# Optimization experiments

Hardware: AMD Instinct MI355X
Metric: run time of the kernel (lower is better)

The kernel has to match this reference:

```python
import jax, jax.numpy as jnp
import numpy as np

H = 128      # hidden_size
ATT = 128    # attention_size
NS = 1024    # num attendee statements
NE = 512     # num attendee eres
M = 1024     # num attenders


def setup_inputs() -> dict:
    key = jax.random.key(0)
    ks = jax.random.split(key, 16)
    s = 1.0 / np.sqrt(H)
    return {
        'attendee_stmts': jax.random.normal(ks[0], (NS, H), jnp.float32),
        'attendee_eres': jax.random.normal(ks[1], (NE, H), jnp.float32),
        'attender': jax.random.normal(ks[2], (M, H), jnp.float32),
        # Score stmt_to_stmt (concat): Linear(2H->H) then Linear(H->1)
        'Wc_s': jax.random.normal(ks[3], (H, 2 * H), jnp.float32) * s,
        'bc_s': jax.random.normal(ks[4], (H,), jnp.float32) * s,
        'ws_s': jax.random.normal(ks[5], (H,), jnp.float32) * s,
        'bs_s': jax.random.normal(ks[6], (1,), jnp.float32) * s,
        # Score ere_to_stmt (concat)
        'Wc_e': jax.random.normal(ks[7], (H, 2 * H), jnp.float32) * s,
        'bc_e': jax.random.normal(ks[8], (H,), jnp.float32) * s,
        'ws_e': jax.random.normal(ks[9], (H,), jnp.float32) * s,
        'bs_e': jax.random.normal(ks[10], (1,), jnp.float32) * s,
        # Attention combine: Linear(3H -> ATT)
        'W_lin': jax.random.normal(ks[11], (ATT, 3 * H), jnp.float32) * s,
        'b_lin': jax.random.normal(ks[12], (ATT,), jnp.float32) * s,
        # coherence_linear: Linear(ATT -> 1)
        'W_coh': jax.random.normal(ks[13], (1, ATT), jnp.float32) * s,
        'b_coh': jax.random.normal(ks[14], (1,), jnp.float32) * s,
    }


def _concat_score(first, second, Wc, bc, ws, bs):
    # torch: single(tanh(concat(cat([first_i, second_j])))) over all (i, j)
    # split concat weight so we never materialize the [N, M, 2H] concat
    h = first.shape[-1]
    A = first @ Wc[:, :h].T + bc          # [N, H]
    B = second @ Wc[:, h:].T              # [M, H]
    Hnm = jnp.tanh(A[:, None, :] + B[None, :, :])   # [N, M, H]
    return jnp.einsum('nmh,h->nm', Hnm, ws) + bs[0]  # [N, M]


def reference(attendee_stmts, attendee_eres, attender,
              Wc_s, bc_s, ws_s, bs_s,
              Wc_e, bc_e, ws_e, bs_e,
              W_lin, b_lin, W_coh, b_coh):
    # unnormalized scores, softmax over attendees (dim 0)
    w_ss = jax.nn.softmax(_concat_score(attendee_stmts, attender, Wc_s, bc_s, ws_s, bs_s), axis=0)  # [NS, M]
    w_es = jax.nn.softmax(_concat_score(attendee_eres, attender, Wc_e, bc_e, ws_e, bs_e), axis=0)   # [NE, M]
    # context vectors: weights^T @ attendees
    ctx_s = jnp.einsum('nm,nh->mh', w_ss, attendee_stmts)  # [M, H]
    ctx_e = jnp.einsum('nm,nh->mh', w_es, attendee_eres)   # [M, H]
    feats = jnp.concatenate([attender, ctx_s, ctx_e], axis=-1)  # [M, 3H]
    att_vec = jnp.tanh(feats @ W_lin.T + b_lin)                 # [M, ATT]
    coherence = att_vec @ W_coh.T + b_coh                       # [M, 1]
    return coherence
```

## Files before the change

### kernel.cpp

```cpp
#include <hip/hip_runtime.h>
#include <math.h>

#define H   128
#define NS  1024
#define NE  512
#define M   1024
#define K2  2.8853900817779268f

__device__ __forceinline__ float exp2_fast(float x) {
#if __has_builtin(__builtin_amdgcn_exp2f)
    return __builtin_amdgcn_exp2f(x);
#else
    return __expf(x * 0.6931471805599453f);
#endif
}

__device__ __forceinline__ float fast_tanh(float x) {
    float e = __expf(2.0f * x);
    float r = __builtin_amdgcn_rcpf(1.0f + e);
    return 1.0f - 2.0f * r;
}

__global__ __launch_bounds__(256) void k_tr(const float* __restrict__ Wc_s,
                                            const float* __restrict__ Wc_e,
                                            const float* __restrict__ W_lin,
                                            float* __restrict__ WT_s1, float* __restrict__ WT_s2,
                                            float* __restrict__ WT_e1, float* __restrict__ WT_e2,
                                            float* __restrict__ WT_lin) {
    int idx = blockIdx.x * 256 + threadIdx.x;
    if (idx < 65536) {
        int t = idx >> 14, r = idx & 16383, k = r >> 7, hh = r & 127;
        const float* src = (t < 2) ? Wc_s : Wc_e;
        int off = (t & 1) * H;
        float v = K2 * src[hh * 256 + off + k];
        float* dst = (t == 0) ? WT_s1 : (t == 1) ? WT_s2 : (t == 2) ? WT_e1 : WT_e2;
        dst[r] = v;
    } else {
        int j2 = idx - 65536;
        int k = j2 >> 7, a = j2 & 127;
        WT_lin[j2] = W_lin[a * 384 + k];
    }
}

__global__ __launch_bounds__(256) void k_proj(const float* __restrict__ stmts,
                                              const float* __restrict__ eres,
                                              const float* __restrict__ attender,
                                              const float* __restrict__ WT_s1,
                                              const float* __restrict__ WT_s2,
                                              const float* __restrict__ WT_e1,
                                              const float* __restrict__ WT_e2,
                                              const float* __restrict__ bc_s,
                                              const float* __restrict__ bc_e,
                                              float* __restrict__ EAT_s, float* __restrict__ EB_s,
                                              float* __restrict__ EAT_e, float* __restrict__ EB_e) {
    __shared__ float xr[16][H];
    __shared__ float red[16][H];
    int b   = blockIdx.x;
    int tid = threadIdx.x;
    int t    = tid & 127;
    int half = tid >> 7;

    if (b < 96) {
        const float *X, *WT, *bias; float* OT; int r0, N;
        if (b < 64) { X = stmts; WT = WT_s1; bias = bc_s; OT = EAT_s; r0 = b * 16;        N = NS; }
        else        { X = eres;  WT = WT_e1; bias = bc_e; OT = EAT_e; r0 = (b - 64) * 16; N = NE; }
        for (int i = tid; i < 16 * H; i += 256) xr[i >> 7][i & 127] = X[(r0 + (i >> 7)) * H + (i & 127)];
        __syncthreads();
        float b0 = (half == 0) ? K2 * bias[t] : 0.0f;
        float acc[16];
        #pragma unroll
        for (int r = 0; r < 16; ++r) acc[r] = b0;
        int k0 = half * 64;
        #pragma unroll 4
        for (int k = k0; k < k0 + 64; ++k) {
            float wv = WT[k * H + t];
            #pragma unroll
            for (int r = 0; r < 16; ++r) acc[r] += xr[r][k] * wv;
        }
        if (half) {
            #pragma unroll
            for (int r = 0; r < 16; ++r) red[r][t] = acc[r];
        }
        __syncthreads();
        if (!half) {
            #pragma unroll
            for (int r = 0; r < 16; ++r) xr[r][t] = exp2_fast(acc[r] + red[r][t]);
        }
        __syncthreads();
        {
            int hh  = tid >> 1;
            int seg = (tid & 1) * 8;
            float4 v0 = make_float4(xr[seg + 0][hh], xr[seg + 1][hh], xr[seg + 2][hh], xr[seg + 3][hh]);
            float4 v1 = make_float4(xr[seg + 4][hh], xr[seg + 5][hh], xr[seg + 6][hh], xr[seg + 7][hh]);
            *(float4*)(OT + (size_t)hh * N + r0 + seg)     = v0;
            *(float4*)(OT + (size_t)hh * N + r0 + seg + 4) = v1;
        }
    } else {
        int b2 = b - 96;
        const float* WT = (b2 < 256) ? WT_s2 : WT_e2;
        float* O        = (b2 < 256) ? EB_s : EB_e;
        int r0          = (b2 & 255) * 4;
        float* xf = &xr[0][0];
        xf[tid]       = attender[r0 * H + tid];
        xf[tid + 256] = attender[r0 * H + 256 + tid];
        __syncthreads();
        float acc[4] = {0.f, 0.f, 0.f, 0.f};
        int k0 = half * 64;
        #pragma unroll 8
        for (int k = k0; k < k0 + 64; ++k) {
            float wv = WT[k * H + t];
            #pragma unroll
            for (int r = 0; r < 4; ++r) acc[r] += xf[r * H + k] * wv;
        }
        if (half) {
            #pragma unroll
            for (int r = 0; r < 4; ++r) red[r][t] = acc[r];
        }
        __syncthreads();
        if (!half) {
            #pragma unroll
            for (int r = 0; r < 4; ++r) O[(r0 + r) * H + t] = exp2_fast(acc[r] + red[r][t]);
        }
    }
}

#define PAIR(eax, eay, ebx, eby, wx, wy, accv)                 \
    { float q0 = fmaf(eax, ebx, 1.0f);                         \
      float q1 = fmaf(eay, eby, 1.0f);                         \
      float nn = wx * q1; nn = fmaf(wy, q0, nn);               \
      float rr = __builtin_amdgcn_rcpf(q0 * q1);               \
      accv = fmaf(nn, rr, accv); }

__global__ __launch_bounds__(512, 4) void k_score_w(const float* __restrict__ EAT_s,
                                                    const float* __restrict__ EB_s,
                                                    const float* __restrict__ ws_s,
                                                    const float* __restrict__ EAT_e,
                                                    const float* __restrict__ EB_e,
                                                    const float* __restrict__ ws_e,
                                                    float* __restrict__ w_s, float* __restrict__ rz_s,
                                                    float* __restrict__ w_e, float* __restrict__ rz_e) {
    __shared__ float Bs[4][H];
    __shared__ float scrm[8][4], scrs[8][4];
    int b = blockIdx.x;
    bool is_e = (b >= 256);
    int m0 = (is_e ? (b - 256) : b) * 4;
    const float* EAT = is_e ? EAT_e : EAT_s;
    const float* EB  = is_e ? EB_e  : EB_s;
    const float* wsv = is_e ? ws_e  : ws_s;
    float* wout      = is_e ? w_e   : w_s;
    float* rzout     = is_e ? rz_e  : rz_s;
    int N    = is_e ? NE : NS;
    int ROWS = is_e ? 1 : 2;
    int t = threadIdx.x;

    Bs[t >> 7][t & 127] = EB[(size_t)(m0 + (t >> 7)) * H + (t & 127)];
    __syncthreads();

    float acc[2][4] = {{0.f,0.f,0.f,0.f},{0.f,0.f,0.f,0.f}};
    for (int h0 = 0; h0 < H; h0 += 8) {
        float a[2][8];
        #pragma unroll
        for (int i = 0; i < 2; ++i)
            if (i < ROWS) {
                #pragma unroll
                for (int k = 0; k < 8; ++k)
                    a[i][k] = EAT[(size_t)(h0 + k) * N + t + 512 * i];
            }
        float wv[8];
        #pragma unroll
        for (int k = 0; k < 8; ++k) wv[k] = wsv[h0 + k];
        #pragma unroll
        for (int mj = 0; mj < 4; ++mj) {
            float bv[8];
            #pragma unroll
            for (int k = 0; k < 8; ++k) bv[k] = Bs[mj][h0 + k];
            #pragma unroll
            for (int i = 0; i < 2; ++i)
                if (i < ROWS) {
                    PAIR(a[i][0], a[i][1], bv[0], bv[1], wv[0], wv[1], acc[i][mj]);
                    PAIR(a[i][2], a[i][3], bv[2], bv[3], wv[2], wv[3], acc[i][mj]);
                    PAIR(a[i][4], a[i][5], bv[4], bv[5], wv[4], wv[5], acc[i][mj]);
                    PAIR(a[i][6], a[i][7], bv[6], bv[7], wv[6], wv[7], acc[i][mj]);
                }
        }
    }

    int wave = t >> 6;
    float mx[4];
    for (int mj = 0; mj < 4; ++mj) {
        float v = -2.0f * acc[0][mj];
        if (ROWS > 1) v = fmaxf(v, -2.0f * acc[1][mj]);
        mx[mj] = v;
    }
    #pragma unroll
    for (int off = 32; off > 0; off >>= 1)
        for (int mj = 0; mj < 4; ++mj) mx[mj] = fmaxf(mx[mj], __shfl_xor(mx[mj], off, 64));
    if ((t & 63) == 0) {
        for (int mj = 0; mj < 4; ++mj) scrm[wave][mj] = mx[mj];
    }
    __syncthreads();
    for (int mj = 0; mj < 4; ++mj) {
        float r = scrm[0][mj];
        for (int i = 1; i < 8; ++i) r = fmaxf(r, scrm[i][mj]);
        mx[mj] = r;
    }

    float w0[4], w1[4], sm[4];
    for (int mj = 0; mj < 4; ++mj) {
        w0[mj] = __expf(fmaf(-2.0f, acc[0][mj], -mx[mj]));
        sm[mj] = w0[mj];
        if (ROWS > 1) { w1[mj] = __expf(fmaf(-2.0f, acc[1][mj], -mx[mj])); sm[mj] += w1[mj]; }
    }
    #pragma unroll
    for (int off = 32; off > 0; off >>= 1)
        for (int mj = 0; mj < 4; ++mj) sm[mj] += __shfl_xor(sm[mj], off, 64);
    if ((t & 63) == 0) {
        for (int mj = 0; mj < 4; ++mj) scrs[wave][mj] = sm[mj];
    }
    __syncthreads();

    for (int mj = 0; mj < 4; ++mj) {
        __builtin_nontemporal_store(w0[mj], wout + (size_t)(m0 + mj) * N + t);
        if (ROWS > 1)
            __builtin_nontemporal_store(w1[mj], wout + (size_t)(m0 + mj) * N + t + 512);
    }
    if (t < 4) {
        float s = scrs[0][t];
        for (int i = 1; i < 8; ++i) s += scrs[i][t];
        rzout[m0 + t] = __builtin_amdgcn_rcpf(s);
    }
}

#define TMD 4
__global__ __launch_bounds__(1024) void k_ctx_mlp(const float* __restrict__ w_s,
                                                  const float* __restrict__ rz_s,
                                                  const float* __restrict__ w_e,
                                                  const float* __restrict__ rz_e,
                                                  const float* __restrict__ stmts,
                                                  const float* __restrict__ eres,
                                                  const float* __restrict__ attender,
                                                  const float* __restrict__ WT_lin,
                                                  const float* __restrict__ b_lin,
                                                  const float* __restrict__ W_coh,
                                                  const float* __restrict__ b_coh,
                                                  float* __restrict__ out) {
    __shared__ float wls[1024][TMD];
    __shared__ float part[8][TMD][H];
    __shared__ float feats[TMD][3 * H];
    __shared__ float redv[512];
    __shared__ float red8[8];
    int m0  = blockIdx.x * TMD;
    int tid = threadIdx.x;
    int h   = tid & (H - 1);
    int g   = tid >> 7;

    float rzs[TMD], rze[TMD];
    #pragma unroll
    for (int j = 0; j < TMD; ++j) { rzs[j] = rz_s[m0 + j]; rze[j] = rz_e[m0 + j]; }

    if (tid < TMD * H) feats[tid >> 7][tid & 127] = attender[(size_t)(m0 + (tid >> 7)) * H + (tid & 127)];

    float vws[TMD], vwe[TMD];
    #pragma unroll
    for (int j = 0; j < TMD; ++j)
        vws[j] = __builtin_nontemporal_load(w_s + (size_t)(m0 + j) * NS + tid);
    if (tid < 512) {
        #pragma unroll
        for (int j = 0; j < TMD; ++j)
            vwe[j] = __builtin_nontemporal_load(w_e + (size_t)(m0 + j) * NE + tid);
    }
    *(float4*)&wls[tid][0] = make_float4(vws[0], vws[1], vws[2], vws[3]);
    __syncthreads();

    {
        float acc[TMD] = {0.f, 0.f, 0.f, 0.f};
        const float* Xb = stmts + (size_t)(g * 128) * H + h;
        #pragma unroll 8
        for (int nn = 0; nn < 128; ++nn) {
            float x = Xb[(size_t)nn * H];
            float4 w4 = *(const float4*)&wls[g * 128 + nn][0];
            acc[0] += w4.x * x; acc[1] += w4.y * x;
            acc[2] += w4.z * x; acc[3] += w4.w * x;
        }
        #pragma unroll
        for (int j = 0; j < TMD; ++j) part[g][j][h] = acc[j];
    }
    __syncthreads();
    if (tid < 512) {
        int j = tid >> 7, hh = tid & 127;
        float s = 0.f;
        #pragma unroll
        for (int gg = 0; gg < 8; ++gg) s += part[gg][j][hh];
        feats[j][H + hh] = s * rzs[j];
    }
    __syncthreads();

    if (tid < 512) *(float4*)&wls[tid][0] = make_float4(vwe[0], vwe[1], vwe[2], vwe[3]);
    __syncthreads();
    {
        float acc[TMD] = {0.f, 0.f, 0.f, 0.f};
        const float* Xb = eres + (size_t)(g * 64) * H + h;
        #pragma unroll 8
        for (int nn = 0; nn < 64; ++nn) {
            float x = Xb[(size_t)nn * H];
            float4 w4 = *(const float4*)&wls[g * 64 + nn][0];
            acc[0] += w4.x * x; acc[1] += w4.y * x;
            acc[2] += w4.z * x; acc[3] += w4.w * x;
        }
        #pragma unroll
        for (int j = 0; j < TMD; ++j) part[g][j][h] = acc[j];
    }
    __syncthreads();
    if (tid < 512) {
        int j = tid >> 7, hh = tid & 127;
        float s = 0.f;
        #pragma unroll
        for (int gg = 0; gg < 8; ++gg) s += part[gg][j][hh];
        feats[j][2 * H + hh] = s * rze[j];
    }
    __syncthreads();

    {
        int a    = tid & 127;
        int jm   = (tid >> 7) & 3;
        int half = tid >> 9;
        float acc = half ? 0.f : b_lin[a];
        int k0 = half * 192;
        #pragma unroll 8
        for (int k = k0; k < k0 + 192; ++k)
            acc += feats[jm][k] * WT_lin[k * H + a];
        if (half) redv[tid & 511] = acc;
        __syncthreads();
        if (!half) {
            acc += redv[tid];
            float v = fast_tanh(acc) * W_coh[a];
            #pragma unroll
            for (int off = 32; off > 0; off >>= 1) v += __shfl_down(v, off, 64);
            if ((tid & 63) == 0) red8[tid >> 6] = v;
        }
        __syncthreads();
        if (tid < TMD) out[m0 + tid] = red8[2 * tid] + red8[2 * tid + 1] + b_coh[0];
    }
}

extern "C" void kernel_launch(void* const* d_in, const int* in_sizes, int n_in,
                              void* d_out, int out_size, void* d_ws, size_t ws_size,
                              hipStream_t stream) {
    const float* stmts    = (const float*)d_in[0];
    const float* eres     = (const float*)d_in[1];
    const float* attender = (const float*)d_in[2];
    const float* Wc_s     = (const float*)d_in[3];
    const float* bc_s     = (const float*)d_in[4];
    const float* ws_s     = (const float*)d_in[5];
    const float* Wc_e     = (const float*)d_in[7];
    const float* bc_e     = (const float*)d_in[8];
    const float* ws_e     = (const float*)d_in[9];
    const float* W_lin    = (const float*)d_in[11];
    const float* b_lin    = (const float*)d_in[12];
    const float* W_coh    = (const float*)d_in[13];
    const float* b_coh    = (const float*)d_in[14];
    float* out = (float*)d_out;

    float* ws    = (float*)d_ws;
    float* WT_s1 = ws;
    float* WT_s2 = WT_s1 + H * H;
    float* WT_e1 = WT_s2 + H * H;
    float* WT_e2 = WT_e1 + H * H;
    float* WT_li = WT_e2 + H * H;
    float* EAT_s = WT_li + 3 * H * H;
    float* EB_s  = EAT_s + NS * H;
    float* EAT_e = EB_s + M * H;
    float* EB_e  = EAT_e + NE * H;
    float* wbs   = EB_e + M * H;
    float* wbe   = wbs + (size_t)M * NS;
    float* rzs   = wbe + (size_t)M * NE;
    float* rze   = rzs + M;

    k_tr<<<448, 256, 0, stream>>>(Wc_s, Wc_e, W_lin, WT_s1, WT_s2, WT_e1, WT_e2, WT_li);
    k_proj<<<608, 256, 0, stream>>>(stmts, eres, attender, WT_s1, WT_s2, WT_e1, WT_e2,
                                    bc_s, bc_e, EAT_s, EB_s, EAT_e, EB_e);
    k_score_w<<<512, 512, 0, stream>>>(EAT_s, EB_s, ws_s, EAT_e, EB_e, ws_e,
                                       wbs, rzs, wbe, rze);
    k_ctx_mlp<<<M / TMD, 1024, 0, stream>>>(wbs, rzs, wbe, rze, stmts, eres, attender,
                                            WT_li, b_lin, W_coh, b_coh, out);
}
```

Measured before the change: 67.75 us.

## Fuse context accumulation into score kernel and split out MLP

The score kernel now keeps the unnormalized softmax weights in shared memory and computes the context vectors directly. This avoids writing and re-reading the full M×N weight matrices through global memory. A separate small MLP kernel reads attender plus both contexts and produces coherence. The score loop also prefetches the next chunk of EAT values while computing the current one. In exchange it uses more shared memory per block (about 24KB), which may reduce occupancy under the 4-blocks launch bound.

```diff
diff --git a/kernel.cpp b/kernel.cpp
--- a/kernel.cpp
+++ b/kernel.cpp
@@ -131,24 +131,29 @@
       float rr = __builtin_amdgcn_rcpf(q0 * q1);               \
       accv = fmaf(nn, rr, accv); }
 
-__global__ __launch_bounds__(512, 4) void k_score_w(const float* __restrict__ EAT_s,
-                                                    const float* __restrict__ EB_s,
-                                                    const float* __restrict__ ws_s,
-                                                    const float* __restrict__ EAT_e,
-                                                    const float* __restrict__ EB_e,
-                                                    const float* __restrict__ ws_e,
-                                                    float* __restrict__ w_s, float* __restrict__ rz_s,
-                                                    float* __restrict__ w_e, float* __restrict__ rz_e) {
+__global__ __launch_bounds__(512, 4) void k_score_ctx(const float* __restrict__ EAT_s,
+                                                      const float* __restrict__ EB_s,
+                                                      const float* __restrict__ ws_s,
+                                                      const float* __restrict__ EAT_e,
+                                                      const float* __restrict__ EB_e,
+                                                      const float* __restrict__ ws_e,
+                                                      const float* __restrict__ stmts,
+                                                      const float* __restrict__ eres,
+                                                      float* __restrict__ ctx_s,
+                                                      float* __restrict__ ctx_e) {
     __shared__ float Bs[4][H];
-    __shared__ float scrm[8][4], scrs[8][4];
+    __shared__ float wbuf[1024][4];
+    __shared__ float part[4][4][H];
+    __shared__ float scrm[8][4], scrs[8][4], rzl[4];
+
     int b = blockIdx.x;
     bool is_e = (b >= 256);
     int m0 = (is_e ? (b - 256) : b) * 4;
     const float* EAT = is_e ? EAT_e : EAT_s;
     const float* EB  = is_e ? EB_e  : EB_s;
     const float* wsv = is_e ? ws_e  : ws_s;
-    float* wout      = is_e ? w_e   : w_s;
-    float* rzout     = is_e ? rz_e  : rz_s;
+    const float* X   = is_e ? eres  : stmts;
+    float* ctxout    = is_e ? ctx_e : ctx_s;
     int N    = is_e ? NE : NS;
     int ROWS = is_e ? 1 : 2;
     int t = threadIdx.x;
@@ -157,15 +162,25 @@
     __syncthreads();
 
     float acc[2][4] = {{0.f,0.f,0.f,0.f},{0.f,0.f,0.f,0.f}};
-    for (int h0 = 0; h0 < H; h0 += 8) {
-        float a[2][8];
-        #pragma unroll
-        for (int i = 0; i < 2; ++i)
-            if (i < ROWS) {
+    float a[2][8];
+    #pragma unroll
+    for (int k = 0; k < 8; ++k) a[0][k] = EAT[(size_t)k * N + t];
+    if (ROWS > 1) {
+        #pragma unroll
+        for (int k = 0; k < 8; ++k) a[1][k] = EAT[(size_t)k * N + t + 512];
+    }
+    #pragma unroll
+    for (int ch = 0; ch < 16; ++ch) {
+        int h0 = ch * 8;
+        float an[2][8];
+        if (ch < 15) {
+            #pragma unroll
+            for (int k = 0; k < 8; ++k) an[0][k] = EAT[(size_t)(h0 + 8 + k) * N + t];
+            if (ROWS > 1) {
                 #pragma unroll
-                for (int k = 0; k < 8; ++k)
-                    a[i][k] = EAT[(size_t)(h0 + k) * N + t + 512 * i];
+                for (int k = 0; k < 8; ++k) an[1][k] = EAT[(size_t)(h0 + 8 + k) * N + t + 512];
             }
+        }
         float wv[8];
         #pragma unroll
         for (int k = 0; k < 8; ++k) wv[k] = wsv[h0 + k];
@@ -174,14 +189,24 @@
             float bv[8];
             #pragma unroll
             for (int k = 0; k < 8; ++k) bv[k] = Bs[mj][h0 + k];
-            #pragma unroll
-            for (int i = 0; i < 2; ++i)
-                if (i < ROWS) {
-                    PAIR(a[i][0], a[i][1], bv[0], bv[1], wv[0], wv[1], acc[i][mj]);
-                    PAIR(a[i][2], a[i][3], bv[2], bv[3], wv[2], wv[3], acc[i][mj]);
-                    PAIR(a[i][4], a[i][5], bv[4], bv[5], wv[4], wv[5], acc[i][mj]);
-                    PAIR(a[i][6], a[i][7], bv[6], bv[7], wv[6], wv[7], acc[i][mj]);
-                }
+            PAIR(a[0][0], a[0][1], bv[0], bv[1], wv[0], wv[1], acc[0][mj]);
+            PAIR(a[0][2], a[0][3], bv[2], bv[3], wv[2], wv[3], acc[0][mj]);
+            PAIR(a[0][4], a[0][5], bv[4], bv[5], wv[4], wv[5], acc[0][mj]);
+            PAIR(a[0][6], a[0][7], bv[6], bv[7], wv[6], wv[7], acc[0][mj]);
+            if (ROWS > 1) {
+                PAIR(a[1][0], a[1][1], bv[0], bv[1], wv[0], wv[1], acc[1][mj]);
+                PAIR(a[1][2], a[1][3], bv[2], bv[3], wv[2], wv[3], acc[1][mj]);
+                PAIR(a[1][4], a[1][5], bv[4], bv[5], wv[4], wv[5], acc[1][mj]);
+                PAIR(a[1][6], a[1][7], bv[6], bv[7], wv[6], wv[7], acc[1][mj]);
+            }
+        }
+        if (ch < 15) {
+            #pragma unroll
+            for (int k = 0; k < 8; ++k) a[0][k] = an[0][k];
+            if (ROWS > 1) {
+                #pragma unroll
+                for (int k = 0; k < 8; ++k) a[1][k] = an[1][k];
+            }
         }
     }
 
@@ -217,130 +242,79 @@
     if ((t & 63) == 0) {
         for (int mj = 0; mj < 4; ++mj) scrs[wave][mj] = sm[mj];
     }
-    __syncthreads();
 
     for (int mj = 0; mj < 4; ++mj) {
-        __builtin_nontemporal_store(w0[mj], wout + (size_t)(m0 + mj) * N + t);
-        if (ROWS > 1)
-            __builtin_nontemporal_store(w1[mj], wout + (size_t)(m0 + mj) * N + t + 512);
-    }
+        wbuf[t][mj] = w0[mj];
+        if (ROWS > 1) wbuf[t + 512][mj] = w1[mj];
+    }
+    __syncthreads();
     if (t < 4) {
         float s = scrs[0][t];
         for (int i = 1; i < 8; ++i) s += scrs[i][t];
-        rzout[m0 + t] = __builtin_amdgcn_rcpf(s);
-    }
-}
-
-#define TMD 4
-__global__ __launch_bounds__(1024) void k_ctx_mlp(const float* __restrict__ w_s,
-                                                  const float* __restrict__ rz_s,
-                                                  const float* __restrict__ w_e,
-                                                  const float* __restrict__ rz_e,
-                                                  const float* __restrict__ stmts,
-                                                  const float* __restrict__ eres,
-                                                  const float* __restrict__ attender,
-                                                  const float* __restrict__ WT_lin,
-                                                  const float* __restrict__ b_lin,
-                                                  const float* __restrict__ W_coh,
-                                                  const float* __restrict__ b_coh,
-                                                  float* __restrict__ out) {
-    __shared__ float wls[1024][TMD];
-    __shared__ float part[8][TMD][H];
-    __shared__ float feats[TMD][3 * H];
-    __shared__ float redv[512];
-    __shared__ float red8[8];
-    int m0  = blockIdx.x * TMD;
-    int tid = threadIdx.x;
-    int h   = tid & (H - 1);
-    int g   = tid >> 7;
-
-    float rzs[TMD], rze[TMD];
-    #pragma unroll
-    for (int j = 0; j < TMD; ++j) { rzs[j] = rz_s[m0 + j]; rze[j] = rz_e[m0 + j]; }
-
-    if (tid < TMD * H) feats[tid >> 7][tid & 127] = attender[(size_t)(m0 + (tid >> 7)) * H + (tid & 127)];
-
-    float vws[TMD], vwe[TMD];
-    #pragma unroll
-    for (int j = 0; j < TMD; ++j)
-        vws[j] = __builtin_nontemporal_load(w_s + (size_t)(m0 + j) * NS + tid);
-    if (tid < 512) {
-        #pragma unroll
-        for (int j = 0; j < TMD; ++j)
-            vwe[j] = __builtin_nontemporal_load(w_e + (size_t)(m0 + j) * NE + tid);
-    }
-    *(float4*)&wls[tid][0] = make_float4(vws[0], vws[1], vws[2], vws[3]);
+        rzl[t] = __builtin_amdgcn_rcpf(s);
+    }
     __syncthreads();
 
     {
-        float acc[TMD] = {0.f, 0.f, 0.f, 0.f};
-        const float* Xb = stmts + (size_t)(g * 128) * H + h;
+        int h = t & 127;
+        int g = t >> 7;
+        int CH = N >> 2;
+        const float* Xb = X + (size_t)(g * CH) * H + h;
+        const float* wb = &wbuf[g * CH][0];
+        float cacc[4] = {0.f, 0.f, 0.f, 0.f};
         #pragma unroll 8
-        for (int nn = 0; nn < 128; ++nn) {
+        for (int nn = 0; nn < CH; ++nn) {
             float x = Xb[(size_t)nn * H];
-            float4 w4 = *(const float4*)&wls[g * 128 + nn][0];
-            acc[0] += w4.x * x; acc[1] += w4.y * x;
-            acc[2] += w4.z * x; acc[3] += w4.w * x;
-        }
-        #pragma unroll
-        for (int j = 0; j < TMD; ++j) part[g][j][h] = acc[j];
-    }
-    __syncthreads();
-    if (tid < 512) {
-        int j = tid >> 7, hh = tid & 127;
-        float s = 0.f;
-        #pragma unroll
-        for (int gg = 0; gg < 8; ++gg) s += part[gg][j][hh];
-        feats[j][H + hh] = s * rzs[j];
-    }
-    __syncthreads();
-
-    if (tid < 512) *(float4*)&wls[tid][0] = make_float4(vwe[0], vwe[1], vwe[2], vwe[3]);
+            float4 w4 = *(const float4*)(wb + nn * 4);
+            cacc[0] += w4.x * x; cacc[1] += w4.y * x;
+            cacc[2] += w4.z * x; cacc[3] += w4.w * x;
+        }
+        #pragma unroll
+        for (int mj = 0; mj < 4; ++mj) part[g][mj][h] = cacc[mj];
+    }
     __syncthreads();
     {
-        float acc[TMD] = {0.f, 0.f, 0.f, 0.f};
-        const float* Xb = eres + (size_t)(g * 64) * H + h;
-        #pragma unroll 8
-        for (int nn = 0; nn < 64; ++nn) {
-            float x = Xb[(size_t)nn * H];
-            float4 w4 = *(const float4*)&wls[g * 64 + nn][0];
-            acc[0] += w4.x * x; acc[1] += w4.y * x;
-            acc[2] += w4.z * x; acc[3] += w4.w * x;
-        }
-        #pragma unroll
-        for (int j = 0; j < TMD; ++j) part[g][j][h] = acc[j];
-    }
-    __syncthreads();
-    if (tid < 512) {
-        int j = tid >> 7, hh = tid & 127;
-        float s = 0.f;
-        #pragma unroll
-        for (int gg = 0; gg < 8; ++gg) s += part[gg][j][hh];
-        feats[j][2 * H + hh] = s * rze[j];
-    }
-    __syncthreads();
-
-    {
-        int a    = tid & 127;
-        int jm   = (tid >> 7) & 3;
-        int half = tid >> 9;
-        float acc = half ? 0.f : b_lin[a];
-        int k0 = half * 192;
-        #pragma unroll 8
-        for (int k = k0; k < k0 + 192; ++k)
-            acc += feats[jm][k] * WT_lin[k * H + a];
-        if (half) redv[tid & 511] = acc;
-        __syncthreads();
-        if (!half) {
-            acc += redv[tid];
-            float v = fast_tanh(acc) * W_coh[a];
-            #pragma unroll
-            for (int off = 32; off > 0; off >>= 1) v += __shfl_down(v, off, 64);
-            if ((tid & 63) == 0) red8[tid >> 6] = v;
-        }
-        __syncthreads();
-        if (tid < TMD) out[m0 + tid] = red8[2 * tid] + red8[2 * tid + 1] + b_coh[0];
-    }
+        int mj = t >> 7, h = t & 127;
+        float s = part[0][mj][h] + part[1][mj][h] + part[2][mj][h] + part[3][mj][h];
+        ctxout[(size_t)(m0 + mj) * H + h] = s * rzl[mj];
+    }
+}
+
+__global__ __launch_bounds__(512) void k_mlp(const float* __restrict__ attender,
+                                             const float* __restrict__ ctx_s,
+                                             const float* __restrict__ ctx_e,
+                                             const float* __restrict__ WT_lin,
+                                             const float* __restrict__ b_lin,
+                                             const float* __restrict__ W_coh,
+                                             const float* __restrict__ b_coh,
+                                             float* __restrict__ out) {
+    __shared__ float feats[4][3 * H];
+    __shared__ float red2[8];
+    int m0 = blockIdx.x * 4;
+    int t  = threadIdx.x;
+
+    for (int i = t; i < 4 * 3 * H; i += 512) {
+        int r = i / (3 * H), c = i % (3 * H);
+        float v;
+        if (c < H)            v = attender[(size_t)(m0 + r) * H + c];
+        else if (c < 2 * H)   v = ctx_s[(size_t)(m0 + r) * H + (c - H)];
+        else                  v = ctx_e[(size_t)(m0 + r) * H + (c - 2 * H)];
+        feats[r][c] = v;
+    }
+    __syncthreads();
+
+    int a  = t & 127;
+    int jm = t >> 7;
+    float acc = b_lin[a];
+    #pragma unroll 8
+    for (int k = 0; k < 3 * H; ++k)
+        acc += feats[jm][k] * WT_lin[k * H + a];
+    float v = fast_tanh(acc) * W_coh[a];
+    #pragma unroll
+    for (int off = 32; off > 0; off >>= 1) v += __shfl_down(v, off, 64);
+    if ((t & 63) == 0) red2[t >> 6] = v;
+    __syncthreads();
+    if (t < 4) out[m0 + t] = red2[2 * t] + red2[2 * t + 1] + b_coh[0];
 }
 
 extern "C" void kernel_launch(void* const* d_in, const int* in_sizes, int n_in,
@@ -371,16 +345,13 @@
     float* EB_s  = EAT_s + NS * H;
     float* EAT_e = EB_s + M * H;
     float* EB_e  = EAT_e + NE * H;
-    float* wbs   = EB_e + M * H;
-    float* wbe   = wbs + (size_t)M * NS;
-    float* rzs   = wbe + (size_t)M * NE;
-    float* rze   = rzs + M;
+    float* c_s   = EB_e + M * H;
+    float* c_e   = c_s + (size_t)M * H;
 
     k_tr<<<448, 256, 0, stream>>>(Wc_s, Wc_e, W_lin, WT_s1, WT_s2, WT_e1, WT_e2, WT_li);
     k_proj<<<608, 256, 0, stream>>>(stmts, eres, attender, WT_s1, WT_s2, WT_e1, WT_e2,
                                     bc_s, bc_e, EAT_s, EB_s, EAT_e, EB_e);
-    k_score_w<<<512, 512, 0, stream>>>(EAT_s, EB_s, ws_s, EAT_e, EB_e, ws_e,
-                                       wbs, rzs, wbe, rze);
-    k_ctx_mlp<<<M / TMD, 1024, 0, stream>>>(wbs, rzs, wbe, rze, stmts, eres, attender,
-                                            WT_li, b_lin, W_coh, b_coh, out);
-}
+    k_score_ctx<<<512, 512, 0, stream>>>(EAT_s, EB_s, ws_s, EAT_e, EB_e, ws_e,
+                                         stmts, eres, c_s, c_e);
+    k_mlp<<<M / 4, 512, 0, stream>>>(attender, c_s, c_e, WT_li, b_lin, W_coh, b_coh, out);
+}
```

New measurement: 67.88 us. About the same (+0.2%).
